# Optimization experiments

Measured on AMD Instinct MI355X. Metric: run time of the kernel, lower is better.

The kernel has to match this reference:

```python
import jax, jax.numpy as jnp
import numpy as np

MODES = 2
LC = 4
N = 6000
KNN = 10
NODES = 64
CH = MODES ** 2
M = N * 2 * (KNN + 1)  # total candidate couplings


def setup_inputs() -> dict:
    key = jax.random.key(0)
    ks = jax.random.split(key, 6)
    return {
        "CK_inputs": jax.random.normal(ks[0], (N, 2 * (KNN + 1), 3), dtype=jnp.float32),
        "W_in": jax.random.normal(ks[1], (3, NODES), dtype=jnp.float32) * 0.1,
        "b_in": jnp.zeros((NODES,), dtype=jnp.float32),
        "W_hid": jax.random.normal(ks[2], (LC - 1, NODES, NODES), dtype=jnp.float32) * 0.1,
        "b_hid": jnp.zeros((LC - 1, NODES), dtype=jnp.float32),
        "W_out": jax.random.normal(ks[3], (NODES, CH), dtype=jnp.float32) * 0.1,
        "b_out": jnp.zeros((CH,), dtype=jnp.float32),
        "coo": jax.random.randint(ks[4], (2, M), 0, N, dtype=jnp.int32),
    }


def _mlp(x, W_in, b_in, W_hid, b_hid, W_out, b_out):
    # MLP: 3 -> 64, (LC-1) hidden 64->64 layers, 64 -> CH; ReLU activations.
    h = jax.nn.relu(x @ W_in + b_in)
    for i in range(W_hid.shape[0]):  # small fixed layer count
        h = jax.nn.relu(h @ W_hid[i] + b_hid[i])
    return h @ W_out + b_out  # [M, CH]


def reference(CK_inputs, W_in, b_in, W_hid, b_hid, W_out, b_out, coo):
    C_stripped = _mlp(CK_inputs.reshape(-1, 3), W_in, b_in, W_hid, b_hid, W_out, b_out)  # [M, CH]
    D = MODES * N
    # Original: for channel ch = mi*MODES+mj, scatter C_stripped[:, ch] at indices coo*MODES+mj
    # (mj added to BOTH row and col, replicating the source exactly). Indices are
    # independent of mi, so sum over mi first, then one scatter-add per mj.
    vals = C_stripped.reshape(-1, MODES, MODES).sum(axis=1)  # [M, MODES]; axis1=mi, axis2=mj
    dense = jnp.zeros((D, D), dtype=CK_inputs.dtype)
    for mj in range(MODES):
        idx = coo * MODES + mj  # [2, M]
        dense = dense.at[idx[0], idx[1]].add(vals[:, mj])
    return dense
```

## Files before the change

kernel.cpp:

```cpp
#include <hip/hip_runtime.h>
#include <stdint.h>

#define NN    6000
#define KNNC  10
#define MM    (NN * 2 * (KNNC + 1))
#define DD    (2 * NN)
#define LCH   3
#define BLK   256

#define FBLOCKS ((MM + 63) / 64)
#define NV      ((long long)DD * DD / 4)

__global__ __launch_bounds__(BLK) void fused_mlp_zero(
    const float* __restrict__ CK,
    const float* __restrict__ Win,
    const float* __restrict__ bin,
    const float* __restrict__ Whid,
    const float* __restrict__ bhid,
    const float* __restrict__ Wout,
    const float* __restrict__ bout,
    float* __restrict__ vals,
    float* __restrict__ out)
{
    __shared__ float sH[64 * 64];

    const int tid  = threadIdx.x;
    const int wave = tid >> 6;
    const int lane = tid & 63;
    const int mlpw = blockIdx.x & 3;

    if (wave != mlpw) {
        const int fw = wave - (wave > mlpw ? 1 : 0);
        const long long ft = (long long)blockIdx.x * 192 + fw * 64 + lane;
        const long long stride = (long long)FBLOCKS * 192;
        float4 z = make_float4(0.f, 0.f, 0.f, 0.f);
        float4* outv = (float4*)out;
        for (long long i = ft; i < NV; i += stride) outv[i] = z;
        return;
    }

    const int m = blockIdx.x * 64 + lane;
    if (m >= MM) return;

    const float x0 = CK[m * 3 + 0];
    const float x1 = CK[m * 3 + 1];
    const float x2 = CK[m * 3 + 2];

    float* __restrict__ hcol = sH + lane;

#pragma unroll
    for (int j = 0; j < 64; j++) {
        float a = bin[j];
        a = fmaf(x0, Win[j],       a);
        a = fmaf(x1, Win[64 + j],  a);
        a = fmaf(x2, Win[128 + j], a);
        hcol[j * 64] = fmaxf(a, 0.0f);
    }

#pragma unroll 1
    for (int l = 0; l < LCH; l++) {
        const float4* __restrict__ W4 = (const float4*)(Whid + (l << 12));
        const float*  __restrict__ bh = bhid + (l << 6);
        float g[64];
#pragma unroll
        for (int j = 0; j < 64; j++) g[j] = bh[j];
#pragma unroll 8
        for (int k = 0; k < 64; k++) {
            const float hk = hcol[k * 64];
            const float4* __restrict__ Wk = W4 + (k << 4);
#pragma unroll
            for (int j4 = 0; j4 < 16; j4++) {
                float4 w = Wk[j4];
                g[j4 * 4 + 0] = fmaf(w.x, hk, g[j4 * 4 + 0]);
                g[j4 * 4 + 1] = fmaf(w.y, hk, g[j4 * 4 + 1]);
                g[j4 * 4 + 2] = fmaf(w.z, hk, g[j4 * 4 + 2]);
                g[j4 * 4 + 3] = fmaf(w.w, hk, g[j4 * 4 + 3]);
            }
        }
#pragma unroll
        for (int j = 0; j < 64; j++) hcol[j * 64] = fmaxf(g[j], 0.0f);
    }

    float v0 = bout[0] + bout[2];
    float v1 = bout[1] + bout[3];
#pragma unroll 8
    for (int k = 0; k < 64; k++) {
        float4 wo = *((const float4*)Wout + k);
        const float hk = hcol[k * 64];
        v0 = fmaf(hk, wo.x + wo.z, v0);
        v1 = fmaf(hk, wo.y + wo.w, v1);
    }
    *(float2*)(vals + 2 * m) = make_float2(v0, v1);
}

__global__ __launch_bounds__(BLK) void scatter_add(
    const float* __restrict__ vals,
    const int* __restrict__ coo,
    float* __restrict__ out)
{
    const int t = blockIdx.x * BLK + threadIdx.x;
    if (t >= MM) return;
    const int r2 = coo[t] * 2;
    const int c2 = coo[MM + t] * 2;
    const float2 v = *(const float2*)(vals + 2 * t);
    const long long f0 = (long long)r2 * DD + c2;
    atomicAdd(out + f0, v.x);
    atomicAdd(out + f0 + DD + 1, v.y);
}

extern "C" void kernel_launch(void* const* d_in, const int* in_sizes, int n_in,
                              void* d_out, int out_size, void* d_ws, size_t ws_size,
                              hipStream_t stream) {
    const float* CK   = (const float*)d_in[0];
    const float* Win  = (const float*)d_in[1];
    const float* bin  = (const float*)d_in[2];
    const float* Whid = (const float*)d_in[3];
    const float* bhid = (const float*)d_in[4];
    const float* Wout = (const float*)d_in[5];
    const float* bout = (const float*)d_in[6];
    const int* coo    = (const int*)d_in[7];
    float* out        = (float*)d_out;
    float* vals       = (float*)d_ws;

    fused_mlp_zero<<<FBLOCKS, BLK, 0, stream>>>(
        CK, Win, bin, Whid, bhid, Wout, bout, vals, out);
    scatter_add<<<(MM + BLK - 1) / BLK, BLK, 0, stream>>>(vals, coo, out);
}
```

Measured before the change: 689.1 us.

## Split MLP and zero-fill work into separate whole blocks interleaved in grid

Instead of each block dedicating one wave to the MLP and three waves to zero-filling the output, the grid now holds dedicated MLP blocks (256 rows each) interleaved one in five with pure fill blocks. This lets fill blocks finish and free resources on their own and gives MLP blocks full occupancy of their own, but MLP blocks now use 64KB of shared memory, which limits how many fit per CU. The last MLP block clamps its row index and masks the store.

```diff
diff --git a/kernel.cpp b/kernel.cpp
--- a/kernel.cpp
+++ b/kernel.cpp
@@ -8,10 +8,12 @@
 #define LCH   3
 #define BLK   256
 
-#define FBLOCKS ((MM + 63) / 64)
-#define NV      ((long long)DD * DD / 4)
+#define NMLPB  516
+#define NFILLB 2064
+#define GRID   (NMLPB + NFILLB)
+#define NV     ((long long)DD * DD / 4)
 
-__global__ __launch_bounds__(BLK) void fused_mlp_zero(
+__global__ __launch_bounds__(BLK) void fill_mlp(
     const float* __restrict__ CK,
     const float* __restrict__ Win,
     const float* __restrict__ bin,
@@ -22,31 +24,30 @@
     float* __restrict__ vals,
     float* __restrict__ out)
 {
-    __shared__ float sH[64 * 64];
+    __shared__ float sH[64 * BLK];
 
-    const int tid  = threadIdx.x;
-    const int wave = tid >> 6;
-    const int lane = tid & 63;
-    const int mlpw = blockIdx.x & 3;
+    const int bid = blockIdx.x;
+    const int tid = threadIdx.x;
+    const int p   = bid % 5;
 
-    if (wave != mlpw) {
-        const int fw = wave - (wave > mlpw ? 1 : 0);
-        const long long ft = (long long)blockIdx.x * 192 + fw * 64 + lane;
-        const long long stride = (long long)FBLOCKS * 192;
+    if (p != 2) {
+        const int fid = (bid / 5) * 4 + p - (p > 2 ? 1 : 0);
+        long long i = (long long)fid * BLK + tid;
+        const long long stride = (long long)NFILLB * BLK;
         float4 z = make_float4(0.f, 0.f, 0.f, 0.f);
         float4* outv = (float4*)out;
-        for (long long i = ft; i < NV; i += stride) outv[i] = z;
+        for (; i < NV; i += stride) outv[i] = z;
         return;
     }
 
-    const int m = blockIdx.x * 64 + lane;
-    if (m >= MM) return;
+    const int m0 = (bid / 5) * BLK + tid;
+    const int m  = m0 < MM ? m0 : MM - 1;
 
     const float x0 = CK[m * 3 + 0];
     const float x1 = CK[m * 3 + 1];
     const float x2 = CK[m * 3 + 2];
 
-    float* __restrict__ hcol = sH + lane;
+    float* __restrict__ hcol = sH + tid;
 
 #pragma unroll
     for (int j = 0; j < 64; j++) {
@@ -54,7 +55,7 @@
         a = fmaf(x0, Win[j],       a);
         a = fmaf(x1, Win[64 + j],  a);
         a = fmaf(x2, Win[128 + j], a);
-        hcol[j * 64] = fmaxf(a, 0.0f);
+        hcol[j * BLK] = fmaxf(a, 0.0f);
     }
 
 #pragma unroll 1
@@ -66,7 +67,7 @@
         for (int j = 0; j < 64; j++) g[j] = bh[j];
 #pragma unroll 8
         for (int k = 0; k < 64; k++) {
-            const float hk = hcol[k * 64];
+            const float hk = hcol[k * BLK];
             const float4* __restrict__ Wk = W4 + (k << 4);
 #pragma unroll
             for (int j4 = 0; j4 < 16; j4++) {
@@ -78,7 +79,7 @@
             }
         }
 #pragma unroll
-        for (int j = 0; j < 64; j++) hcol[j * 64] = fmaxf(g[j], 0.0f);
+        for (int j = 0; j < 64; j++) hcol[j * BLK] = fmaxf(g[j], 0.0f);
     }
 
     float v0 = bout[0] + bout[2];
@@ -86,11 +87,11 @@
 #pragma unroll 8
     for (int k = 0; k < 64; k++) {
         float4 wo = *((const float4*)Wout + k);
-        const float hk = hcol[k * 64];
+        const float hk = hcol[k * BLK];
         v0 = fmaf(hk, wo.x + wo.z, v0);
         v1 = fmaf(hk, wo.y + wo.w, v1);
     }
-    *(float2*)(vals + 2 * m) = make_float2(v0, v1);
+    if (m0 < MM) *(float2*)(vals + 2 * m0) = make_float2(v0, v1);
 }
 
 __global__ __launch_bounds__(BLK) void scatter_add(
@@ -122,7 +123,7 @@
     float* out        = (float*)d_out;
     float* vals       = (float*)d_ws;
 
-    fused_mlp_zero<<<FBLOCKS, BLK, 0, stream>>>(
+    fill_mlp<<<GRID, BLK, 0, stream>>>(
         CK, Win, bin, Whid, bhid, Wout, bout, vals, out);
     scatter_add<<<(MM + BLK - 1) / BLK, BLK, 0, stream>>>(vals, coo, out);
 }
```

Measured after the change: 717.7 us. 1.04x slower.

## Rebalance fused fill/MLP block roles and use unsafe atomic adds in scatter

Applied to the files above, without the earlier changes.

Each block now runs two MLP waves and two zero-fill waves instead of one MLP wave and three fill waves. The grid shrinks to 1032 blocks and wave roles rotate by block index. Out-of-range MLP lanes are clamped rather than returning early. The scatter switches to unsafeAtomicAdd, which lets the compiler emit hardware float atomics instead of CAS loops, at the cost of relying on memory-type-dependent atomic semantics. The intent is to cut the number of blocks and balance MLP compute against the memory-bound 576MB zero fill, and to make the atomics cheaper.

```diff
diff --git a/kernel.cpp b/kernel.cpp
--- a/kernel.cpp
+++ b/kernel.cpp
@@ -8,10 +8,11 @@
 #define LCH   3
 #define BLK   256
 
-#define FBLOCKS ((MM + 63) / 64)
-#define NV      ((long long)DD * DD / 4)
+#define FB    1032
+#define NV    ((long long)DD * DD / 4)
+#define SCGRID ((MM + BLK - 1) / BLK)
 
-__global__ __launch_bounds__(BLK) void fused_mlp_zero(
+__global__ __launch_bounds__(BLK) void fused_fill_mlp(
     const float* __restrict__ CK,
     const float* __restrict__ Win,
     const float* __restrict__ bin,
@@ -22,31 +23,32 @@
     float* __restrict__ vals,
     float* __restrict__ out)
 {
-    __shared__ float sH[64 * 64];
+    __shared__ float sH[2][64 * 64];
 
     const int tid  = threadIdx.x;
     const int wave = tid >> 6;
     const int lane = tid & 63;
-    const int mlpw = blockIdx.x & 3;
+    const int role = (wave + blockIdx.x) & 3;
 
-    if (wave != mlpw) {
-        const int fw = wave - (wave > mlpw ? 1 : 0);
-        const long long ft = (long long)blockIdx.x * 192 + fw * 64 + lane;
-        const long long stride = (long long)FBLOCKS * 192;
+    if (role >= 2) {
+        const int fw = role - 2;
+        const long long ft = ((long long)blockIdx.x * 2 + fw) * 64 + lane;
+        const long long stride = (long long)FB * 2 * 64;
         float4 z = make_float4(0.f, 0.f, 0.f, 0.f);
         float4* outv = (float4*)out;
         for (long long i = ft; i < NV; i += stride) outv[i] = z;
         return;
     }
 
-    const int m = blockIdx.x * 64 + lane;
-    if (m >= MM) return;
+    const int mw = role;
+    const int m0 = blockIdx.x * 128 + mw * 64 + lane;
+    const int m  = m0 < MM ? m0 : MM - 1;
 
     const float x0 = CK[m * 3 + 0];
     const float x1 = CK[m * 3 + 1];
     const float x2 = CK[m * 3 + 2];
 
-    float* __restrict__ hcol = sH + lane;
+    float* __restrict__ hcol = sH[mw] + lane;
 
 #pragma unroll
     for (int j = 0; j < 64; j++) {
@@ -90,7 +92,7 @@
         v0 = fmaf(hk, wo.x + wo.z, v0);
         v1 = fmaf(hk, wo.y + wo.w, v1);
     }
-    *(float2*)(vals + 2 * m) = make_float2(v0, v1);
+    if (m0 < MM) *(float2*)(vals + 2 * m0) = make_float2(v0, v1);
 }
 
 __global__ __launch_bounds__(BLK) void scatter_add(
@@ -104,8 +106,8 @@
     const int c2 = coo[MM + t] * 2;
     const float2 v = *(const float2*)(vals + 2 * t);
     const long long f0 = (long long)r2 * DD + c2;
-    atomicAdd(out + f0, v.x);
-    atomicAdd(out + f0 + DD + 1, v.y);
+    unsafeAtomicAdd(out + f0, v.x);
+    unsafeAtomicAdd(out + f0 + DD + 1, v.y);
 }
 
 extern "C" void kernel_launch(void* const* d_in, const int* in_sizes, int n_in,
@@ -122,7 +124,7 @@
     float* out        = (float*)d_out;
     float* vals       = (float*)d_ws;
 
-    fused_mlp_zero<<<FBLOCKS, BLK, 0, stream>>>(
+    fused_fill_mlp<<<FB, BLK, 0, stream>>>(
         CK, Win, bin, Whid, bhid, Wout, bout, vals, out);
-    scatter_add<<<(MM + BLK - 1) / BLK, BLK, 0, stream>>>(vals, coo, out);
+    scatter_add<<<SCGRID, BLK, 0, stream>>>(vals, coo, out);
 }
```

Measured after the change: 723.5 us. 5.0% more time.
